# Performance work log

Hardware: AMD Instinct MI355X
Metric: run time of the kernel (lower is better)

## Reference

```python
import jax, jax.numpy as jnp
import numpy as np

EPS = 1e-5

def _layernorm(x, g, b):
    mu = jnp.mean(x, axis=-1, keepdims=True)
    var = jnp.mean(jnp.square(x - mu), axis=-1, keepdims=True)
    return (x - mu) * jax.lax.rsqrt(var + EPS) * g + b

def setup_inputs() -> dict:
    key = jax.random.key(0)
    ks = jax.random.split(key, 8)
    B, N, D, DFF = 64, 197, 768, 3072
    s = 0.02
    return {
        "x": jax.random.normal(ks[0], (B, N, D), jnp.float32),
        "ln1_g": jnp.ones((D,), jnp.float32),
        "ln1_b": jnp.zeros((D,), jnp.float32),
        "wq": jax.random.normal(ks[1], (D, D), jnp.float32) * s,
        "bq": jnp.zeros((D,), jnp.float32),
        "wk": jax.random.normal(ks[2], (D, D), jnp.float32) * s,
        "bk": jnp.zeros((D,), jnp.float32),
        "wv": jax.random.normal(ks[3], (D, D), jnp.float32) * s,
        "bv": jnp.zeros((D,), jnp.float32),
        "wo": jax.random.normal(ks[4], (D, D), jnp.float32) * s,
        "bo": jnp.zeros((D,), jnp.float32),
        "ln2_g": jnp.ones((D,), jnp.float32),
        "ln2_b": jnp.zeros((D,), jnp.float32),
        "w1": jax.random.normal(ks[5], (D, DFF), jnp.float32) * s,
        "b1": jnp.zeros((DFF,), jnp.float32),
        "w2": jax.random.normal(ks[6], (DFF, D), jnp.float32) * s,
        "b2": jnp.zeros((D,), jnp.float32),
    }

def reference(x, ln1_g, ln1_b, wq, bq, wk, bk, wv, bv, wo, bo,
              ln2_g, ln2_b, w1, b1, w2, b2):
    B, N, D = x.shape
    H = 12
    hd = D // H
    scale = hd ** -0.5
    # layer_norm1 + qkv projection (disable_reuse path: no reuse module)
    h = _layernorm(x, ln1_g, ln1_b)
    q = (h @ wq + bq).reshape(B, N, H, hd) * scale
    k = (h @ wk + bk).reshape(B, N, H, hd)
    v = (h @ wv + bv).reshape(B, N, H, hd)
    # manual bmm attention, full [B,H,N,N] probs materialized & returned
    qk = jnp.einsum('bqhd,bkhd->bhqk', q, k)
    attn_weights = jax.nn.softmax(qk, axis=-1)
    attn = jnp.einsum('bhqk,bkhd->bqhd', attn_weights, v)
    pre_proj = attn.reshape(B, N, D)
    hs = x + (pre_proj @ wo + bo)
    # MLP block
    residual = hs
    h2 = _layernorm(hs, ln2_g, ln2_b)
    h2 = jax.nn.gelu(h2 @ w1 + b1, approximate=False)
    hidden_states = residual + (h2 @ w2 + b2)
    # reuse_start == 'before_mlp': (pre_proj, cache_states=None, hidden, attn_w, qkvs=None, reuse_map=None)
    return (pre_proj, hidden_states, attn_weights)
```

## Files before the change

kernel.cpp:

```cpp
#include <hip/hip_runtime.h>
#include <math.h>

typedef unsigned short u16;
typedef __bf16 bf16x8 __attribute__((ext_vector_type(8)));
typedef float f32x4 __attribute__((ext_vector_type(4)));

#define MROWS 12608
#define NSEQ  197
#define NHEAD 12
#define DMODEL 768

__device__ __forceinline__ u16 f2bf(float f) {
    unsigned u = __float_as_uint(f);
    u += 0x7FFFu + ((u >> 16) & 1u);
    return (u16)(u >> 16);
}
__device__ __forceinline__ float bf2f(u16 v) { return __uint_as_float(((unsigned)v) << 16); }

__device__ __forceinline__ bf16x8 cvt8(const float* p) {
    float4 a = *(const float4*)p;
    float4 b = *(const float4*)(p + 4);
    union { bf16x8 v; u16 s[8]; } t;
    t.s[0] = f2bf(a.x); t.s[1] = f2bf(a.y); t.s[2] = f2bf(a.z); t.s[3] = f2bf(a.w);
    t.s[4] = f2bf(b.x); t.s[5] = f2bf(b.y); t.s[6] = f2bf(b.z); t.s[7] = f2bf(b.w);
    return t.v;
}

__device__ __forceinline__ void g2l16(const u16* g, u16* l) {
    __builtin_amdgcn_global_load_lds((const __attribute__((address_space(1))) unsigned*)g,
                                     (__attribute__((address_space(3))) unsigned*)l,
                                     16, 0, 0);
}

__global__ __launch_bounds__(256) void ln_rows(const float* x,
                                               const float* g,
                                               const float* bta,
                                               u16* o, int Mr) {
    int w = threadIdx.x >> 6, lane = threadIdx.x & 63;
    int row = blockIdx.x * 4 + w;
    if (row >= Mr) return;
    const float* xr = x + (size_t)row * DMODEL;
    float vals[12];
    for (int i = 0; i < 6; ++i) {
        float2 xx = *(const float2*)(xr + i * 128 + lane * 2);
        vals[2 * i] = xx.x; vals[2 * i + 1] = xx.y;
    }
    float s = 0.f;
    for (int i = 0; i < 12; ++i) s += vals[i];
    for (int off = 1; off < 64; off <<= 1) s += __shfl_xor(s, off, 64);
    float mu = s * (1.f / 768.f);
    float v2 = 0.f;
    for (int i = 0; i < 12; ++i) { float d = vals[i] - mu; v2 += d * d; }
    for (int off = 1; off < 64; off <<= 1) v2 += __shfl_xor(v2, off, 64);
    float rstd = rsqrtf(v2 * (1.f / 768.f) + 1e-5f);
    u16* orow = o + (size_t)row * DMODEL;
    for (int i = 0; i < 6; ++i) {
        int c = i * 128 + lane * 2;
        float2 gg = *(const float2*)(g + c);
        float2 bb = *(const float2*)(bta + c);
        float y0 = (vals[2 * i] - mu) * rstd * gg.x + bb.x;
        float y1 = (vals[2 * i + 1] - mu) * rstd * gg.y + bb.y;
        *(unsigned*)(orow + c) = (unsigned)f2bf(y0) | ((unsigned)f2bf(y1) << 16);
    }
}

__global__ __launch_bounds__(256) void wtrans(const float* __restrict__ src,
                                              u16* __restrict__ dst,
                                              int ldsrc, int lddst) {
    __shared__ float t[32][33];
    int c = threadIdx.x & 31, r0 = threadIdx.x >> 5;
    int k0 = blockIdx.x * 32, n0 = blockIdx.y * 32;
#pragma unroll
    for (int i = 0; i < 4; ++i)
        t[r0 + 8 * i][c] = src[(size_t)(k0 + r0 + 8 * i) * ldsrc + n0 + c];
    __syncthreads();
#pragma unroll
    for (int i = 0; i < 4; ++i)
        dst[(size_t)(n0 + r0 + 8 * i) * lddst + k0 + c] = f2bf(t[c][r0 + 8 * i]);
}

template <int BM>
__device__ __forceinline__ void gemm_core(
    const u16* __restrict__ A, const u16* __restrict__ BT,
    int M, int K, int lda, int ldb,
    u16* aS, u16* bS, f32x4 (&acc)[BM / 32][4])
{
    constexpr int MT  = BM / 32;
    constexpr int LPA = BM / 64;
    int tid = threadIdx.x, w = tid >> 6, lane = tid & 63;
    int row0 = blockIdx.x * BM, col0 = blockIdx.y * 128;
    int kk = (lane & 3) * 8, rsub = lane >> 2;

    const u16* aG[LPA]; int lA[LPA];
#pragma unroll
    for (int i = 0; i < LPA; ++i) {
        int sr = (w * LPA + i) * 16 + rsub;
        int gr = row0 + sr; if (gr > M - 1) gr = M - 1;
        aG[i] = A + (size_t)gr * lda + kk;
        lA[i] = (w * LPA + i) * 512;
    }
    const u16* bG[2]; int lB[2];
#pragma unroll
    for (int i = 0; i < 2; ++i) {
        int sc = (w * 2 + i) * 16 + rsub;
        bG[i] = BT + (size_t)(col0 + sc) * ldb + kk;
        lB[i] = (w * 2 + i) * 512;
    }
    int wmB = (w >> 1) * (BM / 2), wnB = (w & 1) * 64;
    int lrow = lane & 15, lq = lane >> 4;

    const f32x4 z = {0.f, 0.f, 0.f, 0.f};
#pragma unroll
    for (int i = 0; i < MT; ++i)
#pragma unroll
        for (int j = 0; j < 4; ++j) acc[i][j] = z;

#pragma unroll
    for (int i = 0; i < LPA; ++i) g2l16(aG[i], aS + lA[i]);
#pragma unroll
    for (int i = 0; i < 2; ++i)  g2l16(bG[i], bS + lB[i]);
    __syncthreads();

    int nt = K >> 5, cur = 0;
    for (int t = 0; t < nt; ++t) {
        int nxt = cur ^ 1;
        if (t + 1 < nt) {
            int ko = (t + 1) << 5;
#pragma unroll
            for (int i = 0; i < LPA; ++i) g2l16(aG[i] + ko, aS + nxt * (BM * 32) + lA[i]);
#pragma unroll
            for (int i = 0; i < 2; ++i)  g2l16(bG[i] + ko, bS + nxt * 4096 + lB[i]);
        }
        const u16* aC = aS + cur * (BM * 32);
        const u16* bC = bS + cur * 4096;
        bf16x8 af[MT], bfr[4];
#pragma unroll
        for (int mt = 0; mt < MT; ++mt)
            af[mt] = *(const bf16x8*)(aC + (wmB + mt * 16 + lrow) * 32 + lq * 8);
#pragma unroll
        for (int n2 = 0; n2 < 4; ++n2)
            bfr[n2] = *(const bf16x8*)(bC + (wnB + n2 * 16 + lrow) * 32 + lq * 8);
#pragma unroll
        for (int mt = 0; mt < MT; ++mt)
#pragma unroll
            for (int n2 = 0; n2 < 4; ++n2)
                acc[mt][n2] = __builtin_amdgcn_mfma_f32_16x16x32_bf16(af[mt], bfr[n2], acc[mt][n2], 0, 0, 0);
        __syncthreads();
        cur = nxt;
    }
}

template <int BM>
__global__ __launch_bounds__(256) void gemm_std(
    const u16* __restrict__ A, const u16* __restrict__ BT,
    float* Cf, u16* Cb, const float* bias, const float* resid,
    int M, int K, int lda, int ldb, int ldc, float scale, int do_gelu)
{
    __shared__ __align__(16) u16 aS[2 * BM * 32];
    __shared__ __align__(16) u16 bS[2 * 128 * 32];
    constexpr int MT = BM / 32;
    f32x4 acc[MT][4];
    gemm_core<BM>(A, BT, M, K, lda, ldb, aS, bS, acc);

    int tid = threadIdx.x, w = tid >> 6, lane = tid & 63;
    int row0 = blockIdx.x * BM, col0 = blockIdx.y * 128;
    int wmB = (w >> 1) * (BM / 2), wnB = (w & 1) * 64;
    int lrow = lane & 15, lq = lane >> 4;
#pragma unroll
    for (int mt = 0; mt < MT; ++mt) {
        int gmb = row0 + wmB + mt * 16 + lq * 4;
#pragma unroll
        for (int n2 = 0; n2 < 4; ++n2) {
            int gc = col0 + wnB + n2 * 16 + lrow;
            float bv = bias ? bias[gc] : 0.f;
            for (int r = 0; r < 4; ++r) {
                int gm = gmb + r;
                if (gm < M) {
                    float v0 = (acc[mt][n2][r] + bv) * scale;
                    if (do_gelu) v0 = 0.5f * v0 * (1.f + erff(v0 * 0.70710678118654752f));
                    if (resid) v0 += resid[(size_t)gm * ldc + gc];
                    if (Cf) Cf[(size_t)gm * ldc + gc] = v0;
                    if (Cb) Cb[(size_t)gm * ldc + gc] = f2bf(v0);
                }
            }
        }
    }
}

__global__ __launch_bounds__(256) void gemm_qkv(
    const u16* __restrict__ A, const u16* __restrict__ BT,
    float* qo, float* ko, u16* vo,
    const float* bq, const float* bk, const float* bvv, int M)
{
    __shared__ __align__(16) u16 aS[2 * 128 * 32];
    __shared__ __align__(16) u16 bS[2 * 128 * 32];
    f32x4 acc[4][4];
    gemm_core<128>(A, BT, M, 768, 768, 768, aS, bS, acc);

    int tid = threadIdx.x, w = tid >> 6, lane = tid & 63;
    int row0 = blockIdx.x * 128, col0 = blockIdx.y * 128;
    int wmB = (w >> 1) * 64, wnB = (w & 1) * 64;
    int lrow = lane & 15, lq = lane >> 4;
#pragma unroll
    for (int mt = 0; mt < 4; ++mt) {
        int gmb = row0 + wmB + mt * 16 + lq * 4;
#pragma unroll
        for (int n2 = 0; n2 < 4; ++n2) {
            int gc = col0 + wnB + n2 * 16 + lrow;
            int j = gc / 768;
            int c = gc - j * 768;
            const float* bp = (j == 0) ? bq : (j == 1) ? bk : bvv;
            float bb = bp[c];
            for (int r = 0; r < 4; ++r) {
                int gm = gmb + r;
                if (gm < M) {
                    float v0 = acc[mt][n2][r] + bb;
                    size_t off = (size_t)gm * 768 + c;
                    if (j == 0)      qo[off] = v0 * 0.125f;
                    else if (j == 1) ko[off] = v0;
                    else             vo[off] = f2bf(v0);
                }
            }
        }
    }
}

__global__ __launch_bounds__(256) void attn_fused(const float* q, const float* k,
                                                  const u16* v, float* attnw,
                                                  float* outf, u16* outb) {
    __shared__ __align__(16) u16 vT[64 * 224];
    __shared__ __align__(16) u16 P[4][16 * 224];
    int bid = blockIdx.x;
    int bh = bid >> 1, mb = bid & 1;
    int b = bh / NHEAD, hh = bh - b * NHEAD;
    int tid = threadIdx.x, w = tid >> 6, lane = tid & 63;
    int lrow = lane & 15, lq = lane >> 4;

    {
        int cg = (tid & 7) * 8;
        int rb = tid >> 3;
        for (int i = 0; i < 7; ++i) {
            int r = rb + i * 32;
            union { uint4 qv; u16 s[8]; } tmp;
            if (r < 197) {
                tmp.qv = *(const uint4*)(v + (size_t)(b * NSEQ + r) * DMODEL + hh * 64 + cg);
            } else {
                tmp.qv.x = tmp.qv.y = tmp.qv.z = tmp.qv.w = 0u;
            }
            for (int j = 0; j < 8; ++j) vT[(cg + j) * 224 + r] = tmp.s[j];
        }
    }
    u16* Pw = &P[w][0];
#pragma unroll
    for (int r = 0; r < 4; ++r) {
        int m = lq * 4 + r;
        Pw[m * 224 + ((208 + lrow) ^ (lq << 3))] = 0;
    }
    __syncthreads();

    size_t pbase = (size_t)bh * (NSEQ * NSEQ);
    int mstart = mb ? 7 : 0;
    int mcount = mb ? 6 : 7;

    for (int round = 0; round < 2; ++round) {
        int mi = round * 4 + w;
        if (mi >= mcount) continue;
        int mtile = mstart + mi;

        int gm0 = mtile * 16 + lrow; int gmq = gm0 > 196 ? 196 : gm0;
        const float* qrow = q + (size_t)(b * NSEQ + gmq) * DMODEL + hh * 64;
        bf16x8 aq0 = cvt8(qrow + lq * 8);
        bf16x8 aq1 = cvt8(qrow + 32 + lq * 8);

        f32x4 s[13];
#pragma unroll
        for (int nt = 0; nt < 13; ++nt) {
            int gn = nt * 16 + lrow; if (gn > 196) gn = 196;
            const float* krow = k + (size_t)(b * NSEQ + gn) * DMODEL + hh * 64;
            bf16x8 bk0 = cvt8(krow + lq * 8);
            bf16x8 bk1 = cvt8(krow + 32 + lq * 8);
            f32x4 a = {0.f, 0.f, 0.f, 0.f};
            a = __builtin_amdgcn_mfma_f32_16x16x32_bf16(aq0, bk0, a, 0, 0, 0);
            a = __builtin_amdgcn_mfma_f32_16x16x32_bf16(aq1, bk1, a, 0, 0, 0);
            s[nt] = a;
        }

        float rls[4];
        bool colbad = (lrow >= 5);
#pragma unroll
        for (int r = 0; r < 4; ++r) {
            float m1 = -1e30f;
#pragma unroll
            for (int nt = 0; nt < 12; ++nt) m1 = fmaxf(m1, s[nt][r]);
            m1 = fmaxf(m1, colbad ? -1e30f : s[12][r]);
            m1 = fmaxf(m1, __shfl_xor(m1, 1, 64));
            m1 = fmaxf(m1, __shfl_xor(m1, 2, 64));
            m1 = fmaxf(m1, __shfl_xor(m1, 4, 64));
            m1 = fmaxf(m1, __shfl_xor(m1, 8, 64));
            float sm = 0.f;
#pragma unroll
            for (int nt = 0; nt < 13; ++nt) {
                float e = __expf(s[nt][r] - m1);
                if (nt == 12 && colbad) e = 0.f;
                s[nt][r] = e;
                sm += e;
            }
            sm += __shfl_xor(sm, 1, 64);
            sm += __shfl_xor(sm, 2, 64);
            sm += __shfl_xor(sm, 4, 64);
            sm += __shfl_xor(sm, 8, 64);
            rls[r] = 1.f / sm;
        }

#pragma unroll
        for (int nt = 0; nt < 13; ++nt) {
            int gc = nt * 16 + lrow;
            bool cok = (gc < 197);
#pragma unroll
            for (int r = 0; r < 4; ++r) {
                float p = s[nt][r] * rls[r];
                s[nt][r] = p;
                int gm = mtile * 16 + lq * 4 + r;
                if (cok && gm < 197)
                    attnw[pbase + (size_t)gm * 197 + gc] = p;
            }
        }
#pragma unroll
        for (int nt = 0; nt < 13; ++nt) {
#pragma unroll
            for (int r = 0; r < 4; ++r) {
                int m = lq * 4 + r;
                Pw[m * 224 + ((nt * 16 + lrow) ^ (lq << 3))] = f2bf(s[nt][r]);
            }
        }

        f32x4 o[4];
        const f32x4 zf = {0.f, 0.f, 0.f, 0.f};
#pragma unroll
        for (int n2 = 0; n2 < 4; ++n2) o[n2] = zf;
#pragma unroll
        for (int ks = 0; ks < 7; ++ks) {
            bf16x8 af = *(const bf16x8*)(Pw + lrow * 224 + ((ks * 32 + lq * 8) ^ ((lrow >> 2) << 3)));
#pragma unroll
            for (int n2 = 0; n2 < 4; ++n2) {
                bf16x8 bv = *(const bf16x8*)(&vT[(n2 * 16 + lrow) * 224 + ks * 32 + lq * 8]);
                o[n2] = __builtin_amdgcn_mfma_f32_16x16x32_bf16(af, bv, o[n2], 0, 0, 0);
            }
        }
#pragma unroll
        for (int n2 = 0; n2 < 4; ++n2) {
            int gcol = hh * 64 + n2 * 16 + lrow;
#pragma unroll
            for (int r = 0; r < 4; ++r) {
                int gm = mtile * 16 + lq * 4 + r;
                if (gm < 197) {
                    size_t off = (size_t)(b * NSEQ + gm) * DMODEL + gcol;
                    outf[off] = o[n2][r];
                    outb[off] = f2bf(o[n2][r]);
                }
            }
        }
    }
}

extern "C" void kernel_launch(void* const* d_in, const int* in_sizes, int n_in,
                              void* d_out, int out_size, void* d_ws, size_t ws_size,
                              hipStream_t stream) {
    const float* x    = (const float*)d_in[0];
    const float* ln1g = (const float*)d_in[1];
    const float* ln1b = (const float*)d_in[2];
    const float* wq   = (const float*)d_in[3];
    const float* bq   = (const float*)d_in[4];
    const float* wk   = (const float*)d_in[5];
    const float* bk   = (const float*)d_in[6];
    const float* wv   = (const float*)d_in[7];
    const float* bv   = (const float*)d_in[8];
    const float* wo   = (const float*)d_in[9];
    const float* bo   = (const float*)d_in[10];
    const float* ln2g = (const float*)d_in[11];
    const float* ln2b = (const float*)d_in[12];
    const float* w1   = (const float*)d_in[13];
    const float* b1   = (const float*)d_in[14];
    const float* w2   = (const float*)d_in[15];
    const float* b2   = (const float*)d_in[16];

    float* out     = (float*)d_out;
    float* preproj = out;
    float* hidden  = out + 9682944;
    float* attnw   = out + 19365888;

    u16* bufA = (u16*)d_ws;
    u16* bufB = bufA + 9682944;

    u16* qkvT = (u16*)attnw;

    long long tailElems = (long long)(ws_size >> 1) - 19365888LL;
    int CH; u16* w1T;
    if (tailElems >= 1179648LL)      { CH = 768; w1T = bufB + 9682944; }
    else if (tailElems >= 786432LL)  { CH = 512; w1T = bufB + 9682944; }
    else                             { CH = 512; w1T = bufB + 6455296; }
    u16* w2T = w1T + (size_t)CH * 768;
    int NCH = 3072 / CH;

    ln_rows<<<3152, 256, 0, stream>>>(x, ln1g, ln1b, bufA, MROWS);
    wtrans<<<dim3(24, 24), 256, 0, stream>>>(wq, qkvT,           768, 768);
    wtrans<<<dim3(24, 24), 256, 0, stream>>>(wk, qkvT + 589824,  768, 768);
    wtrans<<<dim3(24, 24), 256, 0, stream>>>(wv, qkvT + 1179648, 768, 768);
    gemm_qkv<<<dim3(99, 18), 256, 0, stream>>>(bufA, qkvT, preproj, hidden, bufB,
                                               bq, bk, bv, MROWS);
    attn_fused<<<1536, 256, 0, stream>>>(preproj, hidden, bufB, attnw, preproj, bufA);
    wtrans<<<dim3(24, 24), 256, 0, stream>>>(wo, bufB, 768, 768);
    gemm_std<64><<<dim3(197, 6), 256, 0, stream>>>(bufA, bufB, hidden, nullptr, bo, x,
                                                   MROWS, 768, 768, 768, 768, 1.f, 0);
    ln_rows<<<3152, 256, 0, stream>>>(hidden, ln2g, ln2b, bufA, MROWS);
    for (int ci = 0; ci < NCH; ++ci) {
        wtrans<<<dim3(24, CH / 32), 256, 0, stream>>>(w1 + ci * CH, w1T, 3072, 768);
        wtrans<<<dim3(CH / 32, 24), 256, 0, stream>>>(w2 + (size_t)ci * CH * 768, w2T, 768, CH);
        gemm_std<64><<<dim3(197, CH / 128), 256, 0, stream>>>(
            bufA, w1T, nullptr, bufB, b1 + ci * CH, nullptr,
            MROWS, 768, 768, 768, CH, 1.f, 1);
        gemm_std<64><<<dim3(197, 6), 256, 0, stream>>>(
            bufB, w2T, hidden, nullptr, (ci == 0) ? b2 : nullptr, hidden,
            MROWS, CH, CH, CH, 768, 1.f, 0);
    }
}
```

Baseline: 938.1 us.

## Rewrite GEMM core with per-wave private LDS tiles, XOR swizzle, no block barriers

```diff
diff --git a/kernel.cpp b/kernel.cpp
--- a/kernel.cpp
+++ b/kernel.cpp
@@ -11,9 +11,8 @@
 #define DMODEL 768
 
 __device__ __forceinline__ u16 f2bf(float f) {
-    unsigned u = __float_as_uint(f);
-    u += 0x7FFFu + ((u >> 16) & 1u);
-    return (u16)(u >> 16);
+    __bf16 h = (__bf16)f;
+    return __builtin_bit_cast(u16, h);
 }
 __device__ __forceinline__ float bf2f(u16 v) { return __uint_as_float(((unsigned)v) << 16); }
 
@@ -79,95 +78,94 @@
         dst[(size_t)(n0 + r0 + 8 * i) * lddst + k0 + c] = f2bf(t[c][r0 + 8 * i]);
 }
 
-template <int BM>
-__device__ __forceinline__ void gemm_core(
+__device__ __forceinline__ void gemm_core64(
     const u16* __restrict__ A, const u16* __restrict__ BT,
     int M, int K, int lda, int ldb,
-    u16* aS, u16* bS, f32x4 (&acc)[BM / 32][4])
+    u16 (*S)[4][3072],
+    f32x4 (&acc)[2][4])
 {
-    constexpr int MT  = BM / 32;
-    constexpr int LPA = BM / 64;
     int tid = threadIdx.x, w = tid >> 6, lane = tid & 63;
-    int row0 = blockIdx.x * BM, col0 = blockIdx.y * 128;
-    int kk = (lane & 3) * 8, rsub = lane >> 2;
-
-    const u16* aG[LPA]; int lA[LPA];
-#pragma unroll
-    for (int i = 0; i < LPA; ++i) {
-        int sr = (w * LPA + i) * 16 + rsub;
-        int gr = row0 + sr; if (gr > M - 1) gr = M - 1;
-        aG[i] = A + (size_t)gr * lda + kk;
-        lA[i] = (w * LPA + i) * 512;
-    }
-    const u16* bG[2]; int lB[2];
+    int row0 = blockIdx.x * 64, col0 = blockIdx.y * 128;
+    int wm = w >> 1, wn = w & 1;
+    int rsub = lane >> 2;
+    int kch = ((lane & 3) ^ ((lane >> 3) & 3)) * 8;
+
+    const u16* aG[2];
 #pragma unroll
     for (int i = 0; i < 2; ++i) {
-        int sc = (w * 2 + i) * 16 + rsub;
-        bG[i] = BT + (size_t)(col0 + sc) * ldb + kk;
-        lB[i] = (w * 2 + i) * 512;
-    }
-    int wmB = (w >> 1) * (BM / 2), wnB = (w & 1) * 64;
+        int gr = row0 + wm * 32 + i * 16 + rsub;
+        if (gr > M - 1) gr = M - 1;
+        aG[i] = A + (size_t)gr * lda + kch;
+    }
+    const u16* bG[4];
+#pragma unroll
+    for (int j = 0; j < 4; ++j) {
+        int gc = col0 + wn * 64 + j * 16 + rsub;
+        bG[j] = BT + (size_t)gc * ldb + kch;
+    }
+
+    const f32x4 z = {0.f, 0.f, 0.f, 0.f};
+#pragma unroll
+    for (int i = 0; i < 2; ++i)
+#pragma unroll
+        for (int j = 0; j < 4; ++j) acc[i][j] = z;
+
+    u16* sw0 = &S[0][w][0];
+    u16* sw1 = &S[1][w][0];
+
+    g2l16(aG[0], sw0);        g2l16(aG[1], sw0 + 512);
+    g2l16(bG[0], sw0 + 1024); g2l16(bG[1], sw0 + 1536);
+    g2l16(bG[2], sw0 + 2048); g2l16(bG[3], sw0 + 2560);
+    aG[0] += 32; aG[1] += 32;
+    bG[0] += 32; bG[1] += 32; bG[2] += 32; bG[3] += 32;
+
     int lrow = lane & 15, lq = lane >> 4;
-
-    const f32x4 z = {0.f, 0.f, 0.f, 0.f};
-#pragma unroll
-    for (int i = 0; i < MT; ++i)
-#pragma unroll
-        for (int j = 0; j < 4; ++j) acc[i][j] = z;
-
-#pragma unroll
-    for (int i = 0; i < LPA; ++i) g2l16(aG[i], aS + lA[i]);
-#pragma unroll
-    for (int i = 0; i < 2; ++i)  g2l16(bG[i], bS + lB[i]);
-    __syncthreads();
-
-    int nt = K >> 5, cur = 0;
+    int rof = (lq ^ ((lrow >> 1) & 3)) * 8;
+    int nt = K >> 5;
     for (int t = 0; t < nt; ++t) {
-        int nxt = cur ^ 1;
+        u16* cur = (t & 1) ? sw1 : sw0;
         if (t + 1 < nt) {
-            int ko = (t + 1) << 5;
-#pragma unroll
-            for (int i = 0; i < LPA; ++i) g2l16(aG[i] + ko, aS + nxt * (BM * 32) + lA[i]);
-#pragma unroll
-            for (int i = 0; i < 2; ++i)  g2l16(bG[i] + ko, bS + nxt * 4096 + lB[i]);
-        }
-        const u16* aC = aS + cur * (BM * 32);
-        const u16* bC = bS + cur * 4096;
-        bf16x8 af[MT], bfr[4];
-#pragma unroll
-        for (int mt = 0; mt < MT; ++mt)
-            af[mt] = *(const bf16x8*)(aC + (wmB + mt * 16 + lrow) * 32 + lq * 8);
+            u16* nx = (t & 1) ? sw0 : sw1;
+            g2l16(aG[0], nx);        g2l16(aG[1], nx + 512);
+            g2l16(bG[0], nx + 1024); g2l16(bG[1], nx + 1536);
+            g2l16(bG[2], nx + 2048); g2l16(bG[3], nx + 2560);
+            aG[0] += 32; aG[1] += 32;
+            bG[0] += 32; bG[1] += 32; bG[2] += 32; bG[3] += 32;
+            asm volatile("s_waitcnt vmcnt(6)" ::: "memory");
+        } else {
+            asm volatile("s_waitcnt vmcnt(0)" ::: "memory");
+        }
+        __builtin_amdgcn_sched_barrier(0);
+        bf16x8 af[2], bfr[4];
+#pragma unroll
+        for (int mt = 0; mt < 2; ++mt)
+            af[mt] = *(const bf16x8*)(cur + (mt * 16 + lrow) * 32 + rof);
 #pragma unroll
         for (int n2 = 0; n2 < 4; ++n2)
-            bfr[n2] = *(const bf16x8*)(bC + (wnB + n2 * 16 + lrow) * 32 + lq * 8);
-#pragma unroll
-        for (int mt = 0; mt < MT; ++mt)
+            bfr[n2] = *(const bf16x8*)(cur + 1024 + (n2 * 16 + lrow) * 32 + rof);
+#pragma unroll
+        for (int mt = 0; mt < 2; ++mt)
 #pragma unroll
             for (int n2 = 0; n2 < 4; ++n2)
                 acc[mt][n2] = __builtin_amdgcn_mfma_f32_16x16x32_bf16(af[mt], bfr[n2], acc[mt][n2], 0, 0, 0);
-        __syncthreads();
-        cur = nxt;
-    }
-}
-
-template <int BM>
+    }
+}
+
 __global__ __launch_bounds__(256) void gemm_std(
     const u16* __restrict__ A, const u16* __restrict__ BT,
     float* Cf, u16* Cb, const float* bias, const float* resid,
     int M, int K, int lda, int ldb, int ldc, float scale, int do_gelu)
 {
-    __shared__ __align__(16) u16 aS[2 * BM * 32];
-    __shared__ __align__(16) u16 bS[2 * 128 * 32];
-    constexpr int MT = BM / 32;
-    f32x4 acc[MT][4];
-    gemm_core<BM>(A, BT, M, K, lda, ldb, aS, bS, acc);
+    __shared__ __align__(16) u16 S[2][4][3072];
+    f32x4 acc[2][4];
+    gemm_core64(A, BT, M, K, lda, ldb, S, acc);
 
     int tid = threadIdx.x, w = tid >> 6, lane = tid & 63;
-    int row0 = blockIdx.x * BM, col0 = blockIdx.y * 128;
-    int wmB = (w >> 1) * (BM / 2), wnB = (w & 1) * 64;
+    int row0 = blockIdx.x * 64, col0 = blockIdx.y * 128;
+    int wmB = (w >> 1) * 32, wnB = (w & 1) * 64;
     int lrow = lane & 15, lq = lane >> 4;
 #pragma unroll
-    for (int mt = 0; mt < MT; ++mt) {
+    for (int mt = 0; mt < 2; ++mt) {
         int gmb = row0 + wmB + mt * 16 + lq * 4;
 #pragma unroll
         for (int n2 = 0; n2 < 4; ++n2) {
@@ -192,17 +190,16 @@
     float* qo, float* ko, u16* vo,
     const float* bq, const float* bk, const float* bvv, int M)
 {
-    __shared__ __align__(16) u16 aS[2 * 128 * 32];
-    __shared__ __align__(16) u16 bS[2 * 128 * 32];
-    f32x4 acc[4][4];
-    gemm_core<128>(A, BT, M, 768, 768, 768, aS, bS, acc);
+    __shared__ __align__(16) u16 S[2][4][3072];
+    f32x4 acc[2][4];
+    gemm_core64(A, BT, M, 768, 768, 768, S, acc);
 
     int tid = threadIdx.x, w = tid >> 6, lane = tid & 63;
-    int row0 = blockIdx.x * 128, col0 = blockIdx.y * 128;
-    int wmB = (w >> 1) * 64, wnB = (w & 1) * 64;
+    int row0 = blockIdx.x * 64, col0 = blockIdx.y * 128;
+    int wmB = (w >> 1) * 32, wnB = (w & 1) * 64;
     int lrow = lane & 15, lq = lane >> 4;
 #pragma unroll
-    for (int mt = 0; mt < 4; ++mt) {
+    for (int mt = 0; mt < 2; ++mt) {
         int gmb = row0 + wmB + mt * 16 + lq * 4;
 #pragma unroll
         for (int n2 = 0; n2 < 4; ++n2) {
@@ -406,20 +403,20 @@
     wtrans<<<dim3(24, 24), 256, 0, stream>>>(wq, qkvT,           768, 768);
     wtrans<<<dim3(24, 24), 256, 0, stream>>>(wk, qkvT + 589824,  768, 768);
     wtrans<<<dim3(24, 24), 256, 0, stream>>>(wv, qkvT + 1179648, 768, 768);
-    gemm_qkv<<<dim3(99, 18), 256, 0, stream>>>(bufA, qkvT, preproj, hidden, bufB,
-                                               bq, bk, bv, MROWS);
+    gemm_qkv<<<dim3(197, 18), 256, 0, stream>>>(bufA, qkvT, preproj, hidden, bufB,
+                                                bq, bk, bv, MROWS);
     attn_fused<<<1536, 256, 0, stream>>>(preproj, hidden, bufB, attnw, preproj, bufA);
     wtrans<<<dim3(24, 24), 256, 0, stream>>>(wo, bufB, 768, 768);
-    gemm_std<64><<<dim3(197, 6), 256, 0, stream>>>(bufA, bufB, hidden, nullptr, bo, x,
-                                                   MROWS, 768, 768, 768, 768, 1.f, 0);
+    gemm_std<<<dim3(197, 6), 256, 0, stream>>>(bufA, bufB, hidden, nullptr, bo, x,
+                                               MROWS, 768, 768, 768, 768, 1.f, 0);
     ln_rows<<<3152, 256, 0, stream>>>(hidden, ln2g, ln2b, bufA, MROWS);
     for (int ci = 0; ci < NCH; ++ci) {
         wtrans<<<dim3(24, CH / 32), 256, 0, stream>>>(w1 + ci * CH, w1T, 3072, 768);
         wtrans<<<dim3(CH / 32, 24), 256, 0, stream>>>(w2 + (size_t)ci * CH * 768, w2T, 768, CH);
-        gemm_std<64><<<dim3(197, CH / 128), 256, 0, stream>>>(
+        gemm_std<<<dim3(197, CH / 128), 256, 0, stream>>>(
             bufA, w1T, nullptr, bufB, b1 + ci * CH, nullptr,
             MROWS, 768, 768, 768, CH, 1.f, 1);
-        gemm_std<64><<<dim3(197, 6), 256, 0, stream>>>(
+        gemm_std<<<dim3(197, 6), 256, 0, stream>>>(
             bufB, w2T, hidden, nullptr, (ci == 0) ? b2 : nullptr, hidden,
             MROWS, CH, CH, CH, 768, 1.f, 0);
     }
```

New measurement: 1.089 ms. 1.16x slower.
